# Kernel tuning notes

Hardware: AMD Instinct MI355X
Metric: run time of the kernel (lower is better)

## Reference

```python
import jax, jax.numpy as jnp
import numpy as np

N = 4_000_000

def quat_to_rotmat(q):
    # q: (N,4) normalized [w,x,y,z] -> (N,3,3)
    w, x, y, z = q[:, 0], q[:, 1], q[:, 2], q[:, 3]
    R = jnp.stack([
        jnp.stack([1 - 2*y*y - 2*z*z, 2*x*y - 2*w*z,     2*x*z + 2*w*y],     axis=1),
        jnp.stack([2*x*y + 2*w*z,     1 - 2*x*x - 2*z*z, 2*y*z - 2*w*x],     axis=1),
        jnp.stack([2*x*z - 2*w*y,     2*y*z + 2*w*x,     1 - 2*x*x - 2*y*y], axis=1),
    ], axis=1)
    return R

def setup_inputs() -> dict:
    key = jax.random.key(0)
    k1, k2 = jax.random.split(key)
    rotation_raw = jax.random.normal(k1, (N, 4), dtype=jnp.float32)
    scaling_raw = jax.random.normal(k2, (N, 3), dtype=jnp.float32)
    return {"rotation_raw": rotation_raw, "scaling_raw": scaling_raw}

def reference(rotation_raw, scaling_raw):
    # F.normalize(quat, dim=-1)
    q = rotation_raw / jnp.linalg.norm(rotation_raw, axis=-1, keepdims=True)
    R = quat_to_rotmat(q)                      # (N,3,3)
    s = jnp.exp(scaling_raw)                   # (N,3) scaling = exp activation
    RS = R * s[:, None, :]                     # R @ diag(s): scale columns
    cov = jnp.einsum('nik,njk->nij', RS, RS)   # RS @ RS^T
    return cov
```

## Files before the change

kernel.cpp:

```cpp
#include <hip/hip_runtime.h>
#include <hip/hip_bf16.h>


#define TPB 256
#define PPB 512

typedef float v4f __attribute__((ext_vector_type(4)));

static __device__ __forceinline__ void cov_point(
    float w, float x, float y, float z,
    float s0, float s1, float s2, float c[9])
{
    float inv = rsqrtf(w * w + x * x + y * y + z * z);
    w *= inv; x *= inv; y *= inv; z *= inv;

    float r00 = 1.f - 2.f * (y * y + z * z);
    float r01 = 2.f * (x * y - w * z);
    float r02 = 2.f * (x * z + w * y);
    float r10 = 2.f * (x * y + w * z);
    float r11 = 1.f - 2.f * (x * x + z * z);
    float r12 = 2.f * (y * z - w * x);
    float r20 = 2.f * (x * z - w * y);
    float r21 = 2.f * (y * z + w * x);
    float r22 = 1.f - 2.f * (x * x + y * y);

    float t0 = __expf(2.f * s0);
    float t1 = __expf(2.f * s1);
    float t2 = __expf(2.f * s2);

    c[0] = r00 * r00 * t0 + r01 * r01 * t1 + r02 * r02 * t2;
    c[1] = r00 * r10 * t0 + r01 * r11 * t1 + r02 * r12 * t2;
    c[2] = r00 * r20 * t0 + r01 * r21 * t1 + r02 * r22 * t2;
    c[3] = c[1];
    c[4] = r10 * r10 * t0 + r11 * r11 * t1 + r12 * r12 * t2;
    c[5] = r10 * r20 * t0 + r11 * r21 * t1 + r12 * r22 * t2;
    c[6] = c[2];
    c[7] = c[5];
    c[8] = r20 * r20 * t0 + r21 * r21 * t1 + r22 * r22 * t2;
}

__global__ __launch_bounds__(TPB) void gaussian_cov_kernel(
    const float4* __restrict__ rot4,
    const float4* __restrict__ sca4,
    const float*  __restrict__ sca_f,
    v4f* __restrict__ out4,
    float* __restrict__ out_f,
    int n)
{
    __shared__ float lds[PPB * 9];

    const int tid  = threadIdx.x;
    const int base = blockIdx.x * PPB;
    const int n_pt = min(PPB, n - base);

    const bool act0 = (tid < n_pt);
    const bool act1 = (tid + TPB < n_pt);

    float4 qa, qb;
    if (act0) qa = rot4[base + tid];
    if (act1) qb = rot4[base + TPB + tid];

    float*  lsca  = lds;
    float4* lsca4 = (float4*)lds;
    const int nsf = 3 * n_pt;
    const int ns4 = nsf >> 2;
    const float4* gsca4 = sca4 + ((3 * base) >> 2);
    for (int idx = tid; idx < ns4; idx += TPB)
        lsca4[idx] = gsca4[idx];
    if (tid < (nsf & 3))
        lsca[(ns4 << 2) + tid] = sca_f[3 * base + (ns4 << 2) + tid];

    __syncthreads();

    float c0[9], c1[9];
    if (act0)
        cov_point(qa.x, qa.y, qa.z, qa.w,
                  lsca[3 * tid + 0], lsca[3 * tid + 1], lsca[3 * tid + 2], c0);
    if (act1)
        cov_point(qb.x, qb.y, qb.z, qb.w,
                  lsca[3 * (TPB + tid) + 0], lsca[3 * (TPB + tid) + 1],
                  lsca[3 * (TPB + tid) + 2], c1);

    __syncthreads();

    if (act0) {
        #pragma unroll
        for (int m = 0; m < 9; ++m) lds[9 * tid + m] = c0[m];
    }
    if (act1) {
        #pragma unroll
        for (int m = 0; m < 9; ++m) lds[9 * (TPB + tid) + m] = c1[m];
    }

    __syncthreads();

    const int nof = 9 * n_pt;
    const int no4 = nof >> 2;
    const v4f* lout4 = (const v4f*)lds;
    v4f* gout4 = out4 + ((9 * (size_t)base) >> 2);
    for (int idx = tid; idx < no4; idx += TPB)
        __builtin_nontemporal_store(lout4[idx], &gout4[idx]);
    if (tid < (nof & 3))
        out_f[9 * (size_t)base + (no4 << 2) + tid] = lds[(no4 << 2) + tid];
}

extern "C" void kernel_launch(void* const* d_in, const int* in_sizes, int n_in,
                              void* d_out, int out_size, void* d_ws, size_t ws_size,
                              hipStream_t stream) {
    const int n = in_sizes[0] / 4;

    const float4* rot4 = (const float4*)d_in[0];
    const float4* sca4 = (const float4*)d_in[1];
    const float*  scaf = (const float*)d_in[1];
    v4f*   out4 = (v4f*)d_out;
    float* outf = (float*)d_out;

    const int grid = (n + PPB - 1) / PPB;
    gaussian_cov_kernel<<<grid, TPB, 0, stream>>>(rot4, sca4, scaf, out4, outf, n);
}
```

Baseline: 227.5 us.

## Assign adjacent point pairs per thread and stage output per wavefront without block barriers

Each thread now handles two consecutive points and loads their six scale values directly from global memory as three float2 reads, which removes the shared-memory staging of scales. Output staging in shared memory is split into per-wavefront regions, so the three block-wide __syncthreads are replaced by an LDS wait plus a wave barrier before each wave streams its 128 points out with nontemporal stores. This targets barrier stalls and an extra LDS round trip. In exchange, global loads are less coalesced, since each lane reads two float4 quaternions and three float2 values at strided addresses.

```diff
diff --git a/kernel.cpp b/kernel.cpp
--- a/kernel.cpp
+++ b/kernel.cpp
@@ -1,11 +1,11 @@
 #include <hip/hip_runtime.h>
-#include <hip/hip_bf16.h>
 
 
 #define TPB 256
 #define PPB 512
 
 typedef float v4f __attribute__((ext_vector_type(4)));
+typedef float v2f __attribute__((ext_vector_type(2)));
 
 static __device__ __forceinline__ void cov_point(
     float w, float x, float y, float z,
@@ -41,67 +41,77 @@
 
 __global__ __launch_bounds__(TPB) void gaussian_cov_kernel(
     const float4* __restrict__ rot4,
-    const float4* __restrict__ sca4,
-    const float*  __restrict__ sca_f,
+    const v2f*   __restrict__ sca2,
+    const float* __restrict__ sca_f,
     v4f* __restrict__ out4,
     float* __restrict__ out_f,
     int n)
 {
-    __shared__ float lds[PPB * 9];
+    __shared__ float lds[TPB * 18];
 
     const int tid  = threadIdx.x;
+    const int lane = tid & 63;
+    const int wid  = tid >> 6;
     const int base = blockIdx.x * PPB;
     const int n_pt = min(PPB, n - base);
 
-    const bool act0 = (tid < n_pt);
-    const bool act1 = (tid + TPB < n_pt);
+    const int  rp0 = 2 * tid;
+    const int  p0  = base + rp0;
+    const bool a0  = (rp0     < n_pt);
+    const bool a1  = (rp0 + 1 < n_pt);
 
     float4 qa, qb;
-    if (act0) qa = rot4[base + tid];
-    if (act1) qb = rot4[base + TPB + tid];
-
-    float*  lsca  = lds;
-    float4* lsca4 = (float4*)lds;
-    const int nsf = 3 * n_pt;
-    const int ns4 = nsf >> 2;
-    const float4* gsca4 = sca4 + ((3 * base) >> 2);
-    for (int idx = tid; idx < ns4; idx += TPB)
-        lsca4[idx] = gsca4[idx];
-    if (tid < (nsf & 3))
-        lsca[(ns4 << 2) + tid] = sca_f[3 * base + (ns4 << 2) + tid];
-
-    __syncthreads();
+    v2f sA, sB, sC;
+    if (a1) {
+        qa = rot4[p0];
+        qb = rot4[p0 + 1];
+        const v2f* g = sca2 + ((3 * (size_t)base) >> 1) + 3 * (size_t)tid;
+        sA = g[0]; sB = g[1]; sC = g[2];
+    } else if (a0) {
+        qa = rot4[p0];
+        const v2f* g = sca2 + ((3 * (size_t)base) >> 1) + 3 * (size_t)tid;
+        sA = g[0];
+        sB.x = sca_f[3 * (size_t)p0 + 2];
+    }
 
     float c0[9], c1[9];
-    if (act0)
-        cov_point(qa.x, qa.y, qa.z, qa.w,
-                  lsca[3 * tid + 0], lsca[3 * tid + 1], lsca[3 * tid + 2], c0);
-    if (act1)
-        cov_point(qb.x, qb.y, qb.z, qb.w,
-                  lsca[3 * (TPB + tid) + 0], lsca[3 * (TPB + tid) + 1],
-                  lsca[3 * (TPB + tid) + 2], c1);
+    if (a0) cov_point(qa.x, qa.y, qa.z, qa.w, sA.x, sA.y, sB.x, c0);
+    if (a1) cov_point(qb.x, qb.y, qb.z, qb.w, sB.y, sC.x, sC.y, c1);
 
-    __syncthreads();
-
-    if (act0) {
+    float* lw = lds + wid * 1152;
+    if (a0) {
         #pragma unroll
-        for (int m = 0; m < 9; ++m) lds[9 * tid + m] = c0[m];
+        for (int k = 0; k < 9; ++k) lw[18 * lane + k] = c0[k];
     }
-    if (act1) {
+    if (a1) {
         #pragma unroll
-        for (int m = 0; m < 9; ++m) lds[9 * (TPB + tid) + m] = c1[m];
+        for (int k = 0; k < 9; ++k) lw[18 * lane + 9 + k] = c1[k];
     }
 
-    __syncthreads();
+    asm volatile("s_waitcnt lgkmcnt(0)" ::: "memory");
+    __builtin_amdgcn_wave_barrier();
 
-    const int nof = 9 * n_pt;
-    const int no4 = nof >> 2;
-    const v4f* lout4 = (const v4f*)lds;
-    v4f* gout4 = out4 + ((9 * (size_t)base) >> 2);
-    for (int idx = tid; idx < no4; idx += TPB)
-        __builtin_nontemporal_store(lout4[idx], &gout4[idx]);
-    if (tid < (nof & 3))
-        out_f[9 * (size_t)base + (no4 << 2) + tid] = lds[(no4 << 2) + tid];
+    const int n_w = min(max(n_pt - 128 * wid, 0), 128);
+    if (n_w > 0) {
+        const v4f*  lv   = (const v4f*)lw;
+        const size_t ob  = 9 * (size_t)(base + 128 * wid);
+        v4f* gout = out4 + (ob >> 2);
+        if (n_w == 128) {
+            #pragma unroll
+            for (int k = 0; k < 4; ++k)
+                __builtin_nontemporal_store(lv[lane + 64 * k], &gout[lane + 64 * k]);
+            if (lane < 32)
+                __builtin_nontemporal_store(lv[256 + lane], &gout[256 + lane]);
+        } else {
+            const int nf = 9 * n_w;
+            const int n4 = nf >> 2;
+            for (int i = lane; i < n4; i += 64)
+                __builtin_nontemporal_store(lv[i], &gout[i]);
+            const int rem = nf & 3;
+            if (lane < rem)
+                out_f[ob + (size_t)(n4 << 2) + lane] = lw[(n4 << 2) + lane];
+        }
+    }
 }
 
 extern "C" void kernel_launch(void* const* d_in, const int* in_sizes, int n_in,
@@ -110,11 +120,11 @@
     const int n = in_sizes[0] / 4;
 
     const float4* rot4 = (const float4*)d_in[0];
-    const float4* sca4 = (const float4*)d_in[1];
+    const v2f*    sca2 = (const v2f*)d_in[1];
     const float*  scaf = (const float*)d_in[1];
     v4f*   out4 = (v4f*)d_out;
     float* outf = (float*)d_out;
 
     const int grid = (n + PPB - 1) / PPB;
-    gaussian_cov_kernel<<<grid, TPB, 0, stream>>>(rot4, sca4, scaf, out4, outf, n);
+    gaussian_cov_kernel<<<grid, TPB, 0, stream>>>(rot4, sca2, scaf, out4, outf, n);
 }
```

Result: no change. 227.9 us (+0.2%).
